# Kernel optimization log

Measured on AMD Instinct MI355X. Metric: run time of the kernel, lower is better.

## Reference

```python
import jax, jax.numpy as jnp
import numpy as np

# Model config (matches init_kwargs)
B, J, D_IN, D_MODEL, NUM_HEADS, NUM_LAYERS = 1024, 24, 64, 512, 8, 6
A = J + 1  # joints + cls token
LN_EPS = 1e-5


def setup_inputs() -> dict:
    key = jax.random.key(0)
    ks = jax.random.split(key, 14)
    s = 0.02  # weight init scale
    return {
        "x": jax.random.normal(ks[0], (B, J, D_IN), dtype=jnp.float32),
        # per-joint input embeddings: Linear(d_in, d_model) x J
        "We": jax.random.normal(ks[1], (J, D_IN, D_MODEL), dtype=jnp.float32) * s,
        "be": jnp.zeros((J, D_MODEL), dtype=jnp.float32),
        "cls_token": jax.random.normal(ks[2], (D_MODEL,), dtype=jnp.float32),
        # per-layer shared key/value projections
        "Wk": jax.random.normal(ks[3], (NUM_LAYERS, D_MODEL, D_MODEL), dtype=jnp.float32) * s,
        "bk": jnp.zeros((NUM_LAYERS, D_MODEL), dtype=jnp.float32),
        "Wv": jax.random.normal(ks[4], (NUM_LAYERS, D_MODEL, D_MODEL), dtype=jnp.float32) * s,
        "bv": jnp.zeros((NUM_LAYERS, D_MODEL), dtype=jnp.float32),
        # per-layer, PER-JOINT query projections (ModuleList of A linears)
        "Wq": jax.random.normal(ks[5], (NUM_LAYERS, A, D_MODEL, D_MODEL), dtype=jnp.float32) * s,
        "bq": jnp.zeros((NUM_LAYERS, A, D_MODEL), dtype=jnp.float32),
        "Wo": jax.random.normal(ks[6], (NUM_LAYERS, D_MODEL, D_MODEL), dtype=jnp.float32) * s,
        "bo": jnp.zeros((NUM_LAYERS, D_MODEL), dtype=jnp.float32),
        "ln_g": jnp.ones((NUM_LAYERS, D_MODEL), dtype=jnp.float32),
        "ln_b": jnp.zeros((NUM_LAYERS, D_MODEL), dtype=jnp.float32),
    }


def _layernorm(y, g, b):
    m = jnp.mean(y, axis=-1, keepdims=True)
    v = jnp.var(y, axis=-1, keepdims=True)  # ddof=0 matches torch LayerNorm
    return (y - m) * jax.lax.rsqrt(v + LN_EPS) * g + b


def reference(x, We, be, cls_token, Wk, bk, Wv, bv, Wq, bq, Wo, bo, ln_g, ln_b):
    b = x.shape[0]
    depth = D_MODEL // NUM_HEADS
    # per-joint input embedding -> (B, J, D)
    tok = jnp.einsum("bjd,jde->bje", x, We) + be
    cls = jnp.broadcast_to(cls_token[None, None, :], (b, 1, D_MODEL))
    h = jnp.concatenate([cls, tok], axis=1)  # (B, A, D); the seq dim of 1 is dropped

    def split(t):  # (B, A, D) -> (B, H, A, depth)
        return t.reshape(b, A, NUM_HEADS, depth).transpose(0, 2, 1, 3)

    for l in range(NUM_LAYERS):
        k = h @ Wk[l] + bk[l]                                  # (B, A, D)
        v = h @ Wv[l] + bv[l]                                  # (B, A, D)
        q = jnp.einsum("bad,ade->bae", h, Wq[l]) + bq[l]        # per-joint query
        qh, kh, vh = split(q), split(k), split(v)
        scores = jnp.einsum("bhqd,bhkd->bhqk", qh, kh) / jnp.sqrt(jnp.float32(depth))
        w = jax.nn.softmax(scores, axis=-1)                    # (B, H, A, A)
        o = jnp.einsum("bhqk,bhkd->bhqd", w, vh)
        o = o.transpose(0, 2, 1, 3).reshape(b, A, D_MODEL)
        o = o @ Wo[l] + bo[l]
        h = _layernorm(h + o, ln_g[l], ln_b[l])
    return h  # (B, A, D) == inputs[:, 0, :, :] in the torch code
```

## Files before the change

kernel.cpp:

```cpp
#include <hip/hip_runtime.h>

typedef unsigned short u16;
typedef unsigned int u32;
typedef short bf16x8 __attribute__((ext_vector_type(8)));
typedef float f32x4 __attribute__((ext_vector_type(4)));

#define AS1 __attribute__((address_space(1)))
#define AS3 __attribute__((address_space(3)))

__device__ __forceinline__ u16 f2b(float f) {
  u32 u = __float_as_uint(f);
  u += 0x7fffu + ((u >> 16) & 1u);
  return (u16)(u >> 16);
}
__device__ __forceinline__ float b2f(u16 s) {
  return __uint_as_float(((u32)s) << 16);
}

__device__ __forceinline__ void gload16(const u16* g, u16* l) {
  __builtin_amdgcn_global_load_lds((const AS1 void*)g, (AS3 void*)l, 16, 0, 0);
}

__global__ __launch_bounds__(256) void cast_kernel(const float* __restrict__ x,
                                                   u16* __restrict__ xb, int n4) {
  int i = blockIdx.x * 256 + threadIdx.x;
  if (i >= n4) return;
  float4 v = ((const float4*)x)[i];
  ushort4 u;
  u.x = f2b(v.x); u.y = f2b(v.y); u.z = f2b(v.z); u.w = f2b(v.w);
  ((ushort4*)xb)[i] = u;
}

__global__ __launch_bounds__(256) void cls_kernel(const float* __restrict__ cls,
                                                  u16* __restrict__ hb) {
  int i = blockIdx.x * 256 + threadIdx.x;
  int b = i >> 7;
  int e = (i & 127) << 2;
  float4 v = *(const float4*)(cls + e);
  long off = (long)b * (25 * 512) + e;
  ushort4 u;
  u.x = f2b(v.x); u.y = f2b(v.y); u.z = f2b(v.z); u.w = f2b(v.w);
  *(ushort4*)(hb + off) = u;
}

__global__ __launch_bounds__(256) void convT_kernel(const float* __restrict__ src,
                                                    u16* __restrict__ dst,
                                                    int K, int N,
                                                    long src_gstride, long dst_gstride) {
  __shared__ float t[64][65];
  const int k0 = blockIdx.x * 64, n0 = blockIdx.y * 64;
  const float* s = src + (long)blockIdx.z * src_gstride;
  u16* d = dst + (long)blockIdx.z * dst_gstride;
  for (int i = threadIdx.x; i < 4096; i += 256) {
    int r = i >> 6, c = i & 63;
    t[r][c] = s[(long)(k0 + r) * N + n0 + c];
  }
  __syncthreads();
  for (int i = threadIdx.x; i < 4096; i += 256) {
    int r = i >> 6, c = i & 63;
    d[(long)(n0 + r) * K + k0 + c] = f2b(t[c][r]);
  }
}

__global__ __launch_bounds__(256) void convT4_kernel(
    const float* __restrict__ wq, const float* __restrict__ wk,
    const float* __restrict__ wv, const float* __restrict__ wo,
    u16* __restrict__ dq, u16* __restrict__ dk,
    u16* __restrict__ dv, u16* __restrict__ dwo) {
  __shared__ float t[64][65];
  const int z = blockIdx.z;
  const float* src;
  u16* dst;
  if (z < 25)      { src = wq + (long)z * 262144; dst = dq + (long)z * 262144; }
  else if (z == 25){ src = wk; dst = dk; }
  else if (z == 26){ src = wv; dst = dv; }
  else             { src = wo; dst = dwo; }
  const int k0 = blockIdx.x * 64, n0 = blockIdx.y * 64;
  for (int i = threadIdx.x; i < 4096; i += 256) {
    int r = i >> 6, c = i & 63;
    t[r][c] = src[(long)(k0 + r) * 512 + n0 + c];
  }
  __syncthreads();
  for (int i = threadIdx.x; i < 4096; i += 256) {
    int r = i >> 6, c = i & 63;
    dst[(long)(n0 + r) * 512 + k0 + c] = f2b(t[c][r]);
  }
}

__device__ __forceinline__ void gemm_core(u16* As, u16* Bs,
    const u16* Ag, long a_stride, const u16* Wg, const float* biasg,
    u16* Cg, long c_stride, int K, int m0, int n0) {
  const int tid = threadIdx.x;
  const int lane = tid & 63;
  const int wave = tid >> 6;
  const int wr = wave >> 1, wc = wave & 1;

  const int schunk = lane & 7;
  const u16* ga[4];
  const u16* gb[4];
  u16* la[4];
  u16* lb[4];
#pragma unroll
  for (int i = 0; i < 4; ++i) {
    const int r = wave * 32 + i * 8 + (lane >> 3);
    const int csw = (schunk ^ (r & 7)) << 3;
    ga[i] = Ag + (long)(m0 + r) * a_stride + csw;
    gb[i] = Wg + (long)(n0 + r) * K + csw;
    la[i] = &As[(wave * 32 + i * 8) * 64];
    lb[i] = &Bs[(wave * 32 + i * 8) * 64];
  }

  f32x4 acc[4][4];
#pragma unroll
  for (int m = 0; m < 4; ++m)
#pragma unroll
    for (int n = 0; n < 4; ++n) {
      acc[m][n][0] = 0.f; acc[m][n][1] = 0.f;
      acc[m][n][2] = 0.f; acc[m][n][3] = 0.f;
    }

  for (int k0 = 0; k0 < K; k0 += 64) {
    __syncthreads();
#pragma unroll
    for (int i = 0; i < 4; ++i) {
      gload16(ga[i] + k0, la[i]);
      gload16(gb[i] + k0, lb[i]);
    }
    __syncthreads();

#pragma unroll
    for (int kk = 0; kk < 64; kk += 32) {
      const int kb = kk + ((lane >> 4) << 3);
      bf16x8 af[4], bfr[4];
#pragma unroll
      for (int m = 0; m < 4; ++m) {
        const int R = (wr << 6) + (m << 4) + (lane & 15);
        af[m] = *(const bf16x8*)&As[((R << 6) + kb) ^ ((R & 7) << 3)];
      }
#pragma unroll
      for (int n = 0; n < 4; ++n) {
        const int Cc = (wc << 6) + (n << 4) + (lane & 15);
        bfr[n] = *(const bf16x8*)&Bs[((Cc << 6) + kb) ^ ((Cc & 7) << 3)];
      }
#pragma unroll
      for (int m = 0; m < 4; ++m)
#pragma unroll
        for (int n = 0; n < 4; ++n)
          acc[m][n] = __builtin_amdgcn_mfma_f32_16x16x32_bf16(af[m], bfr[n],
                                                              acc[m][n], 0, 0, 0);
    }
  }

  const int lcol = lane & 15;
  const int lrow = (lane >> 4) << 2;
#pragma unroll
  for (int n = 0; n < 4; ++n) {
    const int col = n0 + (wc << 6) + (n << 4) + lcol;
    const float bv = biasg[col];
#pragma unroll
    for (int m = 0; m < 4; ++m) {
      const int row = m0 + (wr << 6) + (m << 4) + lrow;
#pragma unroll
      for (int j = 0; j < 4; ++j) {
        const float val = acc[m][n][j] + bv;
        Cg[(long)(row + j) * c_stride + col] = f2b(val);
      }
    }
  }
}

__global__ __launch_bounds__(256) void gemm_plain(
    const u16* __restrict__ Abase, long a_stride, long a_goff,
    const u16* __restrict__ Wbase, long w_gstride,
    const float* __restrict__ biasbase, long bias_gstride,
    u16* __restrict__ Cb, long c_stride, long c_goff, int K) {
  __shared__ u16 As[128 * 64];
  __shared__ u16 Bs[128 * 64];
  const int g = blockIdx.z;
  gemm_core(As, Bs,
            Abase + (long)g * a_goff, a_stride,
            Wbase + (long)g * w_gstride,
            biasbase + (long)g * bias_gstride,
            Cb + (long)g * c_goff, c_stride, K,
            blockIdx.x * 128, blockIdx.y * 128);
}

__global__ __launch_bounds__(256) void gemm_qkv(
    const u16* __restrict__ hb,
    const u16* __restrict__ wqT, const u16* __restrict__ wkT, const u16* __restrict__ wvT,
    const float* __restrict__ bq, const float* __restrict__ bk, const float* __restrict__ bv,
    u16* __restrict__ qb, u16* __restrict__ kb, u16* __restrict__ vb) {
  __shared__ u16 As[128 * 64];
  __shared__ u16 Bs[128 * 64];
  const int bid = blockIdx.x;
  const u16* Ag; long a_str; const u16* Wg; const float* bg; u16* Cg; long c_str;
  int mt, nt;
  if (bid < 800) {
    const int g = bid >> 5, rem = bid & 31;
    mt = rem >> 2; nt = rem & 3;
    Ag = hb + (long)g * 512; a_str = 12800;
    Wg = wqT + (long)g * 262144; bg = bq + (long)g * 512;
    Cg = qb + (long)g * 512; c_str = 12800;
  } else if (bid < 1600) {
    const int rem = bid - 800;
    mt = rem >> 2; nt = rem & 3;
    Ag = hb; a_str = 512; Wg = wkT; bg = bk; Cg = kb; c_str = 512;
  } else {
    const int rem = bid - 1600;
    mt = rem >> 2; nt = rem & 3;
    Ag = hb; a_str = 512; Wg = wvT; bg = bv; Cg = vb; c_str = 512;
  }
  gemm_core(As, Bs, Ag, a_str, Wg, bg, Cg, c_str, 512, mt * 128, nt * 128);
}

__global__ __launch_bounds__(256) void attn_kernel(const u16* __restrict__ q,
                                                   u16* __restrict__ kio,
                                                   const u16* __restrict__ v) {
  __shared__ u16 ks_[25 * 256];
  __shared__ u16 vs_[25 * 256];
  const int tid = threadIdx.x;
  const int b = blockIdx.x >> 1;
  const int h0 = blockIdx.x & 1;
  const long base = (long)b * 25 * 512;

  for (int i = tid; i < 800; i += 256) {
    const int j = i >> 5, c = i & 31;
    const long goff = base + (long)j * 512 + h0 * 256 + c * 8;
    ((uint4*)ks_)[i] = *(const uint4*)(kio + goff);
    ((uint4*)vs_)[i] = *(const uint4*)(v + goff);
  }
  __syncthreads();

  const int w = tid >> 6;
  const int lane = tid & 63;
  const int qi = lane >> 1;
  const int half = lane & 1;
  if (qi < 25) {
    const int h = h0 * 4 + w;
    const int dslice = w * 64 + half * 32;

    const u16* qrow = q + base + (long)qi * 512 + h * 64 + half * 32;
    float buf[32];
#pragma unroll
    for (int c = 0; c < 4; ++c) {
      uint4 t = *(const uint4*)(qrow + c * 8);
      const u32 tt[4] = {t.x, t.y, t.z, t.w};
#pragma unroll
      for (int e = 0; e < 4; ++e) {
        buf[c * 8 + 2 * e]     = b2f((u16)tt[e]);
        buf[c * 8 + 2 * e + 1] = b2f((u16)(tt[e] >> 16));
      }
    }

    float sc[25];
    float mx = -1e30f;
#pragma unroll
    for (int j = 0; j < 25; ++j) {
      float s = 0.f;
      const u16* kr = &ks_[j * 256 + dslice];
#pragma unroll
      for (int d = 0; d < 32; d += 2) {
        u32 t = *(const u32*)(kr + d);
        s += buf[d] * b2f((u16)t) + buf[d + 1] * b2f((u16)(t >> 16));
      }
      s += __shfl_xor(s, 1);
      s *= 0.125f;
      sc[j] = s;
      mx = fmaxf(mx, s);
    }
    float sum = 0.f;
#pragma unroll
    for (int j = 0; j < 25; ++j) {
      sc[j] = __expf(sc[j] - mx);
      sum += sc[j];
    }
    const float inv = 1.f / sum;

#pragma unroll
    for (int d = 0; d < 32; ++d) buf[d] = 0.f;
#pragma unroll
    for (int j = 0; j < 25; ++j) {
      const float wj = sc[j];
      const u16* vr = &vs_[j * 256 + dslice];
#pragma unroll
      for (int d = 0; d < 32; d += 2) {
        u32 t = *(const u32*)(vr + d);
        buf[d]     += wj * b2f((u16)t);
        buf[d + 1] += wj * b2f((u16)(t >> 16));
      }
    }

    u16* orow = kio + base + (long)qi * 512 + h * 64 + half * 32;
#pragma unroll
    for (int c = 0; c < 4; ++c) {
      uint4 t;
      u32 tt[4];
#pragma unroll
      for (int e = 0; e < 4; ++e)
        tt[e] = (u32)f2b(buf[c * 8 + 2 * e] * inv) |
                ((u32)f2b(buf[c * 8 + 2 * e + 1] * inv) << 16);
      t.x = tt[0]; t.y = tt[1]; t.z = tt[2]; t.w = tt[3];
      *(uint4*)(orow + c * 8) = t;
    }
  }
}

__global__ __launch_bounds__(256) void ln_kernel(u16* hb,
                                                 const u16* __restrict__ o,
                                                 const float* __restrict__ g,
                                                 const float* __restrict__ bta,
                                                 float* fout) {
  const int lane = threadIdx.x & 63;
  const int wave = threadIdx.x >> 6;
  const long row = (long)blockIdx.x * 4 + wave;
  u16* hr = hb + row * 512;
  const u16* orow = o + row * 512;
  const int base = lane << 3;
  uint4 hv4 = *(const uint4*)(hr + base);
  uint4 ov = *(const uint4*)(orow + base);
  const u32 ha[4] = {hv4.x, hv4.y, hv4.z, hv4.w};
  const u32 oa[4] = {ov.x, ov.y, ov.z, ov.w};
  float y[8];
#pragma unroll
  for (int e = 0; e < 4; ++e) {
    y[2 * e]     = b2f((u16)ha[e])         + b2f((u16)oa[e]);
    y[2 * e + 1] = b2f((u16)(ha[e] >> 16)) + b2f((u16)(oa[e] >> 16));
  }
  float s = 0.f, ss = 0.f;
#pragma unroll
  for (int i = 0; i < 8; ++i) { s += y[i]; ss += y[i] * y[i]; }
#pragma unroll
  for (int off = 32; off > 0; off >>= 1) {
    s += __shfl_down(s, off);
    ss += __shfl_down(ss, off);
  }
  s = __shfl(s, 0);
  ss = __shfl(ss, 0);
  const float mean = s * (1.f / 512.f);
  const float var = ss * (1.f / 512.f) - mean * mean;
  const float rinv = rsqrtf(var + 1e-5f);
  float4 g0 = *(const float4*)(g + base);
  float4 g1 = *(const float4*)(g + base + 4);
  float4 b0 = *(const float4*)(bta + base);
  float4 b1 = *(const float4*)(bta + base + 4);
  float r[8];
  r[0] = (y[0] - mean) * rinv * g0.x + b0.x;
  r[1] = (y[1] - mean) * rinv * g0.y + b0.y;
  r[2] = (y[2] - mean) * rinv * g0.z + b0.z;
  r[3] = (y[3] - mean) * rinv * g0.w + b0.w;
  r[4] = (y[4] - mean) * rinv * g1.x + b1.x;
  r[5] = (y[5] - mean) * rinv * g1.y + b1.y;
  r[6] = (y[6] - mean) * rinv * g1.z + b1.z;
  r[7] = (y[7] - mean) * rinv * g1.w + b1.w;
  uint4 hv;
  hv.x = (u32)f2b(r[0]) | ((u32)f2b(r[1]) << 16);
  hv.y = (u32)f2b(r[2]) | ((u32)f2b(r[3]) << 16);
  hv.z = (u32)f2b(r[4]) | ((u32)f2b(r[5]) << 16);
  hv.w = (u32)f2b(r[6]) | ((u32)f2b(r[7]) << 16);
  *(uint4*)(hr + base) = hv;
  if (fout) {
    float* fr = fout + row * 512 + base;
    float4 w0 = {r[0], r[1], r[2], r[3]};
    float4 w1 = {r[4], r[5], r[6], r[7]};
    *(float4*)(fr) = w0;
    *(float4*)(fr + 4) = w1;
  }
}

extern "C" void kernel_launch(void* const* d_in, const int* in_sizes, int n_in,
                              void* d_out, int out_size, void* d_ws, size_t ws_size,
                              hipStream_t stream) {
  const float* x   = (const float*)d_in[0];
  const float* We  = (const float*)d_in[1];
  const float* be  = (const float*)d_in[2];
  const float* cls = (const float*)d_in[3];
  const float* Wk  = (const float*)d_in[4];
  const float* bk  = (const float*)d_in[5];
  const float* Wv  = (const float*)d_in[6];
  const float* bv  = (const float*)d_in[7];
  const float* Wq  = (const float*)d_in[8];
  const float* bq  = (const float*)d_in[9];
  const float* Wo  = (const float*)d_in[10];
  const float* bo  = (const float*)d_in[11];
  const float* lng = (const float*)d_in[12];
  const float* lnb = (const float*)d_in[13];
  float* out = (float*)d_out;

  char* ws = (char*)d_ws;
  u16* hb = (u16*)ws;
  u16* kb = (u16*)(ws + 26214400);
  u16* vb = (u16*)(ws + 52428800);
  u16* qb = (u16*)(ws + 78643200);
  u16* xb = kb;

  u16* scr = (u16*)d_out;
  u16* weT = scr;
  u16* wqT = scr;
  u16* wkT = scr + 6553600;
  u16* wvT = scr + 6815744;
  u16* woT = scr + 7077888;

  cast_kernel<<<1536, 256, 0, stream>>>(x, xb, 393216);
  cls_kernel<<<512, 256, 0, stream>>>(cls, hb);
  convT_kernel<<<dim3(1, 8, 24), 256, 0, stream>>>(We, weT, 64, 512, 32768, 32768);
  gemm_plain<<<dim3(8, 4, 24), 256, 0, stream>>>(
      xb, 1536, 64, weT, 32768, be, 512, hb + 512, 12800, 512, 64);

  for (int l = 0; l < 6; ++l) {
    convT4_kernel<<<dim3(8, 8, 28), 256, 0, stream>>>(
        Wq + (long)l * 6553600, Wk + (long)l * 262144,
        Wv + (long)l * 262144, Wo + (long)l * 262144,
        wqT, wkT, wvT, woT);
    gemm_qkv<<<2400, 256, 0, stream>>>(
        hb, wqT, wkT, wvT,
        bq + (long)l * 12800, bk + (long)l * 512, bv + (long)l * 512,
        qb, kb, vb);
    attn_kernel<<<2048, 256, 0, stream>>>(qb, kb, vb);
    gemm_plain<<<dim3(200, 4, 1), 256, 0, stream>>>(
        kb, 512, 0, woT, 0, bo + (long)l * 512, 0, qb, 512, 0, 512);
    ln_kernel<<<6400, 256, 0, stream>>>(hb, qb, lng + l * 512, lnb + l * 512,
                                        (l == 5) ? out : nullptr);
  }
}
```

Before: 1.113 ms.

## Double-buffer LDS tiles in GEMM core and add occupancy hint to attention

The GEMM main loop now uses two LDS buffers for each of A and B. The async global-to-LDS loads for the next K tile are issued before the MFMA work on the current tile, and one barrier per iteration replaces two, so load latency can overlap with compute. This doubles LDS per block to 64KB, which lowers how many GEMM blocks fit on a CU. Separately, the attention kernel gets a minimum-blocks-per-CU launch bound, which caps register use to raise occupancy.

```diff
diff --git a/kernel.cpp b/kernel.cpp
--- a/kernel.cpp
+++ b/kernel.cpp
@@ -87,9 +87,14 @@
   }
 }
 
-__device__ __forceinline__ void gemm_core(u16* As, u16* Bs,
+__device__ __forceinline__ void gemm_core(u16* lds,
     const u16* Ag, long a_stride, const u16* Wg, const float* biasg,
     u16* Cg, long c_stride, int K, int m0, int n0) {
+  u16* As0 = lds;
+  u16* Bs0 = lds + 8192;
+  u16* As1 = lds + 16384;
+  u16* Bs1 = lds + 24576;
+
   const int tid = threadIdx.x;
   const int lane = tid & 63;
   const int wave = tid >> 6;
@@ -98,16 +103,14 @@
   const int schunk = lane & 7;
   const u16* ga[4];
   const u16* gb[4];
-  u16* la[4];
-  u16* lb[4];
+  int lo[4];
 #pragma unroll
   for (int i = 0; i < 4; ++i) {
     const int r = wave * 32 + i * 8 + (lane >> 3);
     const int csw = (schunk ^ (r & 7)) << 3;
     ga[i] = Ag + (long)(m0 + r) * a_stride + csw;
     gb[i] = Wg + (long)(n0 + r) * K + csw;
-    la[i] = &As[(wave * 32 + i * 8) * 64];
-    lb[i] = &Bs[(wave * 32 + i * 8) * 64];
+    lo[i] = (wave * 32 + i * 8) * 64;
   }
 
   f32x4 acc[4][4];
@@ -119,15 +122,14 @@
       acc[m][n][2] = 0.f; acc[m][n][3] = 0.f;
     }
 
-  for (int k0 = 0; k0 < K; k0 += 64) {
-    __syncthreads();
+  auto STAGE = [&](int k0, u16* A, u16* B) {
 #pragma unroll
     for (int i = 0; i < 4; ++i) {
-      gload16(ga[i] + k0, la[i]);
-      gload16(gb[i] + k0, lb[i]);
-    }
-    __syncthreads();
-
+      gload16(ga[i] + k0, A + lo[i]);
+      gload16(gb[i] + k0, B + lo[i]);
+    }
+  };
+  auto COMPUTE = [&](const u16* A, const u16* B) {
 #pragma unroll
     for (int kk = 0; kk < 64; kk += 32) {
       const int kb = kk + ((lane >> 4) << 3);
@@ -135,12 +137,12 @@
 #pragma unroll
       for (int m = 0; m < 4; ++m) {
         const int R = (wr << 6) + (m << 4) + (lane & 15);
-        af[m] = *(const bf16x8*)&As[((R << 6) + kb) ^ ((R & 7) << 3)];
+        af[m] = *(const bf16x8*)&A[((R << 6) + kb) ^ ((R & 7) << 3)];
       }
 #pragma unroll
       for (int n = 0; n < 4; ++n) {
         const int Cc = (wc << 6) + (n << 4) + (lane & 15);
-        bfr[n] = *(const bf16x8*)&Bs[((Cc << 6) + kb) ^ ((Cc & 7) << 3)];
+        bfr[n] = *(const bf16x8*)&B[((Cc << 6) + kb) ^ ((Cc & 7) << 3)];
       }
 #pragma unroll
       for (int m = 0; m < 4; ++m)
@@ -149,6 +151,21 @@
           acc[m][n] = __builtin_amdgcn_mfma_f32_16x16x32_bf16(af[m], bfr[n],
                                                               acc[m][n], 0, 0, 0);
     }
+  };
+
+  const int nt = K >> 6;
+  STAGE(0, As0, Bs0);
+  __syncthreads();
+  for (int t = 0; t < nt; ++t) {
+    u16* cA = (t & 1) ? As1 : As0;
+    u16* cB = (t & 1) ? Bs1 : Bs0;
+    if (t + 1 < nt) {
+      u16* nA = (t & 1) ? As0 : As1;
+      u16* nB = (t & 1) ? Bs0 : Bs1;
+      STAGE((t + 1) << 6, nA, nB);
+    }
+    COMPUTE(cA, cB);
+    if (t + 1 < nt) __syncthreads();
   }
 
   const int lcol = lane & 15;
@@ -174,10 +191,9 @@
     const u16* __restrict__ Wbase, long w_gstride,
     const float* __restrict__ biasbase, long bias_gstride,
     u16* __restrict__ Cb, long c_stride, long c_goff, int K) {
-  __shared__ u16 As[128 * 64];
-  __shared__ u16 Bs[128 * 64];
+  __shared__ u16 lds[4 * 8192];
   const int g = blockIdx.z;
-  gemm_core(As, Bs,
+  gemm_core(lds,
             Abase + (long)g * a_goff, a_stride,
             Wbase + (long)g * w_gstride,
             biasbase + (long)g * bias_gstride,
@@ -190,8 +206,7 @@
     const u16* __restrict__ wqT, const u16* __restrict__ wkT, const u16* __restrict__ wvT,
     const float* __restrict__ bq, const float* __restrict__ bk, const float* __restrict__ bv,
     u16* __restrict__ qb, u16* __restrict__ kb, u16* __restrict__ vb) {
-  __shared__ u16 As[128 * 64];
-  __shared__ u16 Bs[128 * 64];
+  __shared__ u16 lds[4 * 8192];
   const int bid = blockIdx.x;
   const u16* Ag; long a_str; const u16* Wg; const float* bg; u16* Cg; long c_str;
   int mt, nt;
@@ -210,12 +225,12 @@
     mt = rem >> 2; nt = rem & 3;
     Ag = hb; a_str = 512; Wg = wvT; bg = bv; Cg = vb; c_str = 512;
   }
-  gemm_core(As, Bs, Ag, a_str, Wg, bg, Cg, c_str, 512, mt * 128, nt * 128);
-}
-
-__global__ __launch_bounds__(256) void attn_kernel(const u16* __restrict__ q,
-                                                   u16* __restrict__ kio,
-                                                   const u16* __restrict__ v) {
+  gemm_core(lds, Ag, a_str, Wg, bg, Cg, c_str, 512, mt * 128, nt * 128);
+}
+
+__global__ __launch_bounds__(256, 4) void attn_kernel(const u16* __restrict__ q,
+                                                      u16* __restrict__ kio,
+                                                      const u16* __restrict__ v) {
   __shared__ u16 ks_[25 * 256];
   __shared__ u16 vs_[25 * 256];
   const int tid = threadIdx.x;
```

After: 1.413 ms. 1.27x slower.
